# Kernel optimization log

Hardware: AMD Instinct MI355X
Metric: run time of the kernel (lower is better)

The kernel has to match this reference:

```python
import jax, jax.numpy as jnp
import numpy as np

WINDOW = 33  # must match init_kwargs window_size (odd)


def setup_inputs() -> dict:
    key = jax.random.key(0)
    kq, kk, kv, km = jax.random.split(key, 4)
    B, S, D = 4, 2048, 256
    query = jax.random.normal(kq, (B, S, D), dtype=jnp.float32)
    k = jax.random.normal(kk, (B, S, D), dtype=jnp.float32)
    value = jax.random.normal(kv, (B, S, D), dtype=jnp.float32)
    mask = jax.random.randint(km, (B, S), 0, 2).astype(jnp.int32)
    return {"query": query, "key": k, "value": value, "mask": mask}


def reference(query, key, value, mask):
    # Local (sliding-window) attention, window centered at each position.
    B, S, D = query.shape
    half = WINDOW // 2
    offs = jnp.arange(-half, half + 1)                 # [W]
    idx = jnp.arange(S)[:, None] + offs[None, :]       # [S, W]
    valid = (idx >= 0) & (idx < S)                     # in-bounds window entries
    idxc = jnp.clip(idx, 0, S - 1)
    k_win = key[:, idxc]                               # [B, S, W, D]
    v_win = value[:, idxc]                             # [B, S, W, D]
    scores = jnp.einsum('bsd,bswd->bsw', query, k_win) / jnp.sqrt(jnp.float32(D))
    m_win = (mask[:, idxc] != 0) & valid[None]         # [B, S, W]
    scores = jnp.where(m_win, scores, jnp.float32(-1e10))  # masked_fill(-1e10)
    p_attn = jax.nn.softmax(scores, axis=-1)           # [B, S, W]
    values = jnp.einsum('bsw,bswd->bsd', p_attn, v_win)
    return values, p_attn
```

## Files before the change

kernel.cpp:

```cpp
#include <hip/hip_runtime.h>

#define S_LEN 2048
#define D_DIM 256
#define WIN 33
#define HALF 16
#define TROWS 16
#define SPAN 48
#define SC_STRIDE 68
#define PT_STRIDE 72

typedef __attribute__((ext_vector_type(8))) short short8_t;
typedef __attribute__((ext_vector_type(4))) float f32x4;

__device__ inline unsigned pack2_bf16(float lo, float hi) {
    unsigned a = __float_as_uint(lo) + 0x8000u;
    unsigned b = __float_as_uint(hi) + 0x8000u;
    return __builtin_amdgcn_perm(b, a, 0x07060302);
}
__device__ inline short8_t pack_bf16x8(float4 x, float4 y) {
    union { unsigned u[4]; short8_t s; } r;
    r.u[0] = pack2_bf16(x.x, x.y); r.u[1] = pack2_bf16(x.z, x.w);
    r.u[2] = pack2_bf16(y.x, y.y); r.u[3] = pack2_bf16(y.z, y.w);
    return r.s;
}

__device__ inline void lds_barrier() {
    asm volatile("s_waitcnt lgkmcnt(0)\n\ts_barrier" ::: "memory");
}

__global__ __launch_bounds__(512, 4) void local_attn_v9(
    const float* __restrict__ q,
    const float* __restrict__ k,
    const float* __restrict__ v,
    const int*   __restrict__ mask,
    float* __restrict__ out_v,
    float* __restrict__ out_p)
{
    __shared__ __align__(16) float          Sc[2][TROWS * SC_STRIDE];
    __shared__ __align__(16) unsigned short Pt[TROWS * PT_STRIDE];
    __shared__ int wm[SPAN];

    const int t    = threadIdx.x;
    const int lane = t & 63;
    const int w    = t >> 6;
    const int l15  = lane & 15;
    const int q4   = lane >> 4;

    const int bid  = blockIdx.x;
    const int tile = ((bid & 7) << 6) | (bid >> 3);
    const int b    = tile >> 7;
    const int ts   = tile & 127;
    const int s0   = ts << 4;
    const bool interior = (ts >= 1) && (ts <= 126);

    const float* qb = q + ((size_t)b * S_LEN + s0) * D_DIM;
    const float* kb = k + (size_t)b * S_LEN * D_DIM;
    const float* vb = v + (size_t)b * S_LEN * D_DIM;

    if (t < SPAN) {
        const int idx = s0 - HALF + t;
        wm[t] = (idx >= 0 && idx < S_LEN) ? (mask[b * S_LEN + idx] != 0) : 0;
    }

    float vr[2][2][8];
    const bool act1 = (q4 < 2);

    if (interior) {
        if (w < 6) {
            const int tl = w >> 1;
            const int h  = w & 1;
            const int c  = 16 * tl + l15;
            const float* kr = kb + (size_t)(s0 - HALF + c) * D_DIM;
            const float* qr = qb + (size_t)l15 * D_DIM;
            f32x4 acc = (f32x4){0.f, 0.f, 0.f, 0.f};
#pragma unroll
            for (int i = 0; i < 4; ++i) {
                const int ks = 4 * h + i;
                const float* pq = qr + ks * 32 + q4 * 8;
                const float* pk = kr + ks * 32 + q4 * 8;
                const short8_t aq = pack_bf16x8(*(const float4*)pq, *(const float4*)(pq + 4));
                const short8_t bk = pack_bf16x8(*(const float4*)pk, *(const float4*)(pk + 4));
                acc = __builtin_amdgcn_mfma_f32_16x16x32_bf16(aq, bk, acc, 0, 0, 0);
            }
#pragma unroll
            for (int r = 0; r < 4; ++r)
                Sc[h][(q4 * 4 + r) * SC_STRIDE + c] = acc[r];
        }
        const float* pv = vb + (size_t)(s0 - HALF + q4 * 8) * D_DIM + 32 * w + l15;
#pragma unroll
        for (int nt = 0; nt < 2; ++nt) {
            const float* p0 = pv + nt * 16;
#pragma unroll
            for (int j = 0; j < 8; ++j)
                vr[nt][0][j] = p0[(size_t)j * D_DIM];
            if (act1) {
                const float* p1 = p0 + (size_t)32 * D_DIM;
#pragma unroll
                for (int j = 0; j < 8; ++j)
                    vr[nt][1][j] = p1[(size_t)j * D_DIM];
            }
        }
    } else {
        if (w < 6) {
            const int tl = w >> 1;
            const int h  = w & 1;
            const int c    = 16 * tl + l15;
            const int kidx = min(max(s0 - HALF + c, 0), S_LEN - 1);
            const float* kr = kb + (size_t)kidx * D_DIM;
            const float* qr = qb + (size_t)l15 * D_DIM;
            f32x4 acc = (f32x4){0.f, 0.f, 0.f, 0.f};
#pragma unroll
            for (int i = 0; i < 4; ++i) {
                const int ks = 4 * h + i;
                const float* pq = qr + ks * 32 + q4 * 8;
                const float* pk = kr + ks * 32 + q4 * 8;
                const short8_t aq = pack_bf16x8(*(const float4*)pq, *(const float4*)(pq + 4));
                const short8_t bk = pack_bf16x8(*(const float4*)pk, *(const float4*)(pk + 4));
                acc = __builtin_amdgcn_mfma_f32_16x16x32_bf16(aq, bk, acc, 0, 0, 0);
            }
#pragma unroll
            for (int r = 0; r < 4; ++r)
                Sc[h][(q4 * 4 + r) * SC_STRIDE + c] = acc[r];
        }
#pragma unroll
        for (int nt = 0; nt < 2; ++nt) {
            const int d = 32 * w + nt * 16 + l15;
#pragma unroll
            for (int j = 0; j < 8; ++j) {
                const int g0   = q4 * 8 + j;
                const int idx0 = min(max(s0 - HALF + g0, 0), S_LEN - 1);
                vr[nt][0][j] = vb[(size_t)idx0 * D_DIM + d];
            }
            if (act1) {
#pragma unroll
                for (int j = 0; j < 8; ++j) {
                    const int g1   = 32 + q4 * 8 + j;
                    const int idx1 = min(max(s0 - HALF + g1, 0), S_LEN - 1);
                    vr[nt][1][j] = vb[(size_t)idx1 * D_DIM + d];
                }
            }
        }
    }

    lds_barrier();

    {
        const int row = t >> 5;
        const int e   = t & 31;
        float vs[2];
#pragma unroll
        for (int kq = 0; kq < 2; ++kq) {
            const int c  = 2 * e + kq;
            const int j  = c - row;
            const int cc = (c < SPAN) ? c : 0;
            const bool inb = (j >= 0) && (j < WIN) && (c < SPAN);
            const float sv = (Sc[0][row * SC_STRIDE + cc] + Sc[1][row * SC_STRIDE + cc]) * 0.0625f;
            vs[kq] = inb ? (wm[cc] ? sv : -1e10f) : -1e30f;
        }
        float m = fmaxf(vs[0], vs[1]);
        m = fmaxf(m, __shfl_xor(m, 1, 64));
        m = fmaxf(m, __shfl_xor(m, 2, 64));
        m = fmaxf(m, __shfl_xor(m, 4, 64));
        m = fmaxf(m, __shfl_xor(m, 8, 64));
        m = fmaxf(m, __shfl_xor(m, 16, 64));
        float s = 0.f;
#pragma unroll
        for (int kq = 0; kq < 2; ++kq) { vs[kq] = __expf(vs[kq] - m); s += vs[kq]; }
        s += __shfl_xor(s, 1, 64);
        s += __shfl_xor(s, 2, 64);
        s += __shfl_xor(s, 4, 64);
        s += __shfl_xor(s, 8, 64);
        s += __shfl_xor(s, 16, 64);
        const float rinv = 1.0f / s;

        float p0 = vs[0] * rinv, p1 = vs[1] * rinv;
        *(unsigned*)&Pt[row * PT_STRIDE + 2 * e] = pack2_bf16(p0, p1);
        float* prow = out_p + ((size_t)(b * S_LEN + s0 + row)) * WIN;
        const int j0 = 2 * e - row;
        if (j0 >= 0 && j0 < WIN)         prow[j0]     = p0;
        if (j0 + 1 >= 0 && j0 + 1 < WIN) prow[j0 + 1] = p1;
    }

    lds_barrier();

    {
        const short8_t zfrag = {0, 0, 0, 0, 0, 0, 0, 0};
        short8_t bv[2][2];
#pragma unroll
        for (int nt = 0; nt < 2; ++nt) {
            float4 x, y;
            x.x = vr[nt][0][0]; x.y = vr[nt][0][1]; x.z = vr[nt][0][2]; x.w = vr[nt][0][3];
            y.x = vr[nt][0][4]; y.y = vr[nt][0][5]; y.z = vr[nt][0][6]; y.w = vr[nt][0][7];
            bv[nt][0] = pack_bf16x8(x, y);
            if (act1) {
                x.x = vr[nt][1][0]; x.y = vr[nt][1][1]; x.z = vr[nt][1][2]; x.w = vr[nt][1][3];
                y.x = vr[nt][1][4]; y.y = vr[nt][1][5]; y.z = vr[nt][1][6]; y.w = vr[nt][1][7];
                bv[nt][1] = pack_bf16x8(x, y);
            } else {
                bv[nt][1] = zfrag;
            }
        }

        const short8_t ap0 = *(const short8_t*)&Pt[l15 * PT_STRIDE + q4 * 8];
        const short8_t ap1 = *(const short8_t*)&Pt[l15 * PT_STRIDE + 32 + q4 * 8];
        float* ob = out_v + ((size_t)b * S_LEN + s0) * D_DIM;
#pragma unroll
        for (int nt = 0; nt < 2; ++nt) {
            f32x4 acc = (f32x4){0.f, 0.f, 0.f, 0.f};
            acc = __builtin_amdgcn_mfma_f32_16x16x32_bf16(ap0, bv[nt][0], acc, 0, 0, 0);
            acc = __builtin_amdgcn_mfma_f32_16x16x32_bf16(ap1, bv[nt][1], acc, 0, 0, 0);
            const int d = 32 * w + nt * 16 + l15;
#pragma unroll
            for (int r = 0; r < 4; ++r)
                ob[(size_t)(q4 * 4 + r) * D_DIM + d] = acc[r];
        }
    }
}

extern "C" void kernel_launch(void* const* d_in, const int* in_sizes, int n_in,
                              void* d_out, int out_size, void* d_ws, size_t ws_size,
                              hipStream_t stream) {
    const float* q    = (const float*)d_in[0];
    const float* k    = (const float*)d_in[1];
    const float* v    = (const float*)d_in[2];
    const int*   mask = (const int*)d_in[3];

    const int B = 4;
    float* out_v = (float*)d_out;
    float* out_p = (float*)d_out + (size_t)B * S_LEN * D_DIM;

    const int blocks = B * (S_LEN / TROWS);
    local_attn_v9<<<blocks, 512, 0, stream>>>(q, k, v, mask, out_v, out_p);
}
```

Baseline: 83.30 us.

## Process 32 query rows per block with 1024 threads to share K/V frame

```diff
diff --git a/kernel.cpp b/kernel.cpp
--- a/kernel.cpp
+++ b/kernel.cpp
@@ -4,8 +4,8 @@
 #define D_DIM 256
 #define WIN 33
 #define HALF 16
-#define TROWS 16
-#define SPAN 48
+#define TROWS 32
+#define FRAME 64
 #define SC_STRIDE 68
 #define PT_STRIDE 72
 
@@ -28,7 +28,7 @@
     asm volatile("s_waitcnt lgkmcnt(0)\n\ts_barrier" ::: "memory");
 }
 
-__global__ __launch_bounds__(512, 4) void local_attn_v9(
+__global__ __launch_bounds__(1024, 4) void local_attn_v10(
     const float* __restrict__ q,
     const float* __restrict__ k,
     const float* __restrict__ v,
@@ -38,7 +38,7 @@
 {
     __shared__ __align__(16) float          Sc[2][TROWS * SC_STRIDE];
     __shared__ __align__(16) unsigned short Pt[TROWS * PT_STRIDE];
-    __shared__ int wm[SPAN];
+    __shared__ int wm[FRAME];
 
     const int t    = threadIdx.x;
     const int lane = t & 63;
@@ -47,31 +47,33 @@
     const int q4   = lane >> 4;
 
     const int bid  = blockIdx.x;
-    const int tile = ((bid & 7) << 6) | (bid >> 3);
-    const int b    = tile >> 7;
-    const int ts   = tile & 127;
-    const int s0   = ts << 4;
-    const bool interior = (ts >= 1) && (ts <= 126);
+    const int tile = ((bid & 7) << 5) | (bid >> 3);
+    const int b    = tile >> 6;
+    const int ts   = tile & 63;
+    const int s0   = ts << 5;
+    const bool interior = (ts >= 1) && (ts <= 62);
 
     const float* qb = q + ((size_t)b * S_LEN + s0) * D_DIM;
     const float* kb = k + (size_t)b * S_LEN * D_DIM;
     const float* vb = v + (size_t)b * S_LEN * D_DIM;
 
-    if (t < SPAN) {
+    if (t < FRAME) {
         const int idx = s0 - HALF + t;
         wm[t] = (idx >= 0 && idx < S_LEN) ? (mask[b * S_LEN + idx] != 0) : 0;
     }
 
-    float vr[2][2][8];
-    const bool act1 = (q4 < 2);
+    const int tt = w >> 1;
+    const int h  = w & 1;
+    const int rt = tt >> 2;
+    const int ct = tt & 3;
+    const int c  = 16 * ct + l15;
+
+    float vr[2][8];
 
     if (interior) {
-        if (w < 6) {
-            const int tl = w >> 1;
-            const int h  = w & 1;
-            const int c  = 16 * tl + l15;
+        {
             const float* kr = kb + (size_t)(s0 - HALF + c) * D_DIM;
-            const float* qr = qb + (size_t)l15 * D_DIM;
+            const float* qr = qb + (size_t)(16 * rt + l15) * D_DIM;
             f32x4 acc = (f32x4){0.f, 0.f, 0.f, 0.f};
 #pragma unroll
             for (int i = 0; i < 4; ++i) {
@@ -84,30 +86,21 @@
             }
 #pragma unroll
             for (int r = 0; r < 4; ++r)
-                Sc[h][(q4 * 4 + r) * SC_STRIDE + c] = acc[r];
-        }
-        const float* pv = vb + (size_t)(s0 - HALF + q4 * 8) * D_DIM + 32 * w + l15;
-#pragma unroll
-        for (int nt = 0; nt < 2; ++nt) {
-            const float* p0 = pv + nt * 16;
-#pragma unroll
-            for (int j = 0; j < 8; ++j)
-                vr[nt][0][j] = p0[(size_t)j * D_DIM];
-            if (act1) {
-                const float* p1 = p0 + (size_t)32 * D_DIM;
-#pragma unroll
-                for (int j = 0; j < 8; ++j)
-                    vr[nt][1][j] = p1[(size_t)j * D_DIM];
-            }
-        }
+                Sc[h][(16 * rt + q4 * 4 + r) * SC_STRIDE + c] = acc[r];
+        }
+        const float* pv = vb + (size_t)(s0 - HALF + q4 * 8) * D_DIM + 16 * w + l15;
+#pragma unroll
+        for (int j = 0; j < 8; ++j)
+            vr[0][j] = pv[(size_t)j * D_DIM];
+        const float* pv1 = pv + (size_t)32 * D_DIM;
+#pragma unroll
+        for (int j = 0; j < 8; ++j)
+            vr[1][j] = pv1[(size_t)j * D_DIM];
     } else {
-        if (w < 6) {
-            const int tl = w >> 1;
-            const int h  = w & 1;
-            const int c    = 16 * tl + l15;
+        {
             const int kidx = min(max(s0 - HALF + c, 0), S_LEN - 1);
             const float* kr = kb + (size_t)kidx * D_DIM;
-            const float* qr = qb + (size_t)l15 * D_DIM;
+            const float* qr = qb + (size_t)(16 * rt + l15) * D_DIM;
             f32x4 acc = (f32x4){0.f, 0.f, 0.f, 0.f};
 #pragma unroll
             for (int i = 0; i < 4; ++i) {
@@ -120,26 +113,17 @@
             }
 #pragma unroll
             for (int r = 0; r < 4; ++r)
-                Sc[h][(q4 * 4 + r) * SC_STRIDE + c] = acc[r];
-        }
-#pragma unroll
-        for (int nt = 0; nt < 2; ++nt) {
-            const int d = 32 * w + nt * 16 + l15;
+                Sc[h][(16 * rt + q4 * 4 + r) * SC_STRIDE + c] = acc[r];
+        }
+        const int d = 16 * w + l15;
+#pragma unroll
+        for (int ks = 0; ks < 2; ++ks)
 #pragma unroll
             for (int j = 0; j < 8; ++j) {
-                const int g0   = q4 * 8 + j;
-                const int idx0 = min(max(s0 - HALF + g0, 0), S_LEN - 1);
-                vr[nt][0][j] = vb[(size_t)idx0 * D_DIM + d];
+                const int g   = ks * 32 + q4 * 8 + j;
+                const int idx = min(max(s0 - HALF + g, 0), S_LEN - 1);
+                vr[ks][j] = vb[(size_t)idx * D_DIM + d];
             }
-            if (act1) {
-#pragma unroll
-                for (int j = 0; j < 8; ++j) {
-                    const int g1   = 32 + q4 * 8 + j;
-                    const int idx1 = min(max(s0 - HALF + g1, 0), S_LEN - 1);
-                    vr[nt][1][j] = vb[(size_t)idx1 * D_DIM + d];
-                }
-            }
-        }
     }
 
     lds_barrier();
@@ -150,10 +134,9 @@
         float vs[2];
 #pragma unroll
         for (int kq = 0; kq < 2; ++kq) {
-            const int c  = 2 * e + kq;
-            const int j  = c - row;
-            const int cc = (c < SPAN) ? c : 0;
-            const bool inb = (j >= 0) && (j < WIN) && (c < SPAN);
+            const int cc = 2 * e + kq;
+            const int j  = cc - row;
+            const bool inb = (j >= 0) && (j < WIN);
             const float sv = (Sc[0][row * SC_STRIDE + cc] + Sc[1][row * SC_STRIDE + cc]) * 0.0625f;
             vs[kq] = inb ? (wm[cc] ? sv : -1e10f) : -1e30f;
         }
@@ -184,35 +167,27 @@
     lds_barrier();
 
     {
-        const short8_t zfrag = {0, 0, 0, 0, 0, 0, 0, 0};
-        short8_t bv[2][2];
-#pragma unroll
-        for (int nt = 0; nt < 2; ++nt) {
+        short8_t bv[2];
+#pragma unroll
+        for (int ks = 0; ks < 2; ++ks) {
             float4 x, y;
-            x.x = vr[nt][0][0]; x.y = vr[nt][0][1]; x.z = vr[nt][0][2]; x.w = vr[nt][0][3];
-            y.x = vr[nt][0][4]; y.y = vr[nt][0][5]; y.z = vr[nt][0][6]; y.w = vr[nt][0][7];
-            bv[nt][0] = pack_bf16x8(x, y);
-            if (act1) {
-                x.x = vr[nt][1][0]; x.y = vr[nt][1][1]; x.z = vr[nt][1][2]; x.w = vr[nt][1][3];
-                y.x = vr[nt][1][4]; y.y = vr[nt][1][5]; y.z = vr[nt][1][6]; y.w = vr[nt][1][7];
-                bv[nt][1] = pack_bf16x8(x, y);
-            } else {
-                bv[nt][1] = zfrag;
-            }
-        }
-
-        const short8_t ap0 = *(const short8_t*)&Pt[l15 * PT_STRIDE + q4 * 8];
-        const short8_t ap1 = *(const short8_t*)&Pt[l15 * PT_STRIDE + 32 + q4 * 8];
+            x.x = vr[ks][0]; x.y = vr[ks][1]; x.z = vr[ks][2]; x.w = vr[ks][3];
+            y.x = vr[ks][4]; y.y = vr[ks][5]; y.z = vr[ks][6]; y.w = vr[ks][7];
+            bv[ks] = pack_bf16x8(x, y);
+        }
+
         float* ob = out_v + ((size_t)b * S_LEN + s0) * D_DIM;
-#pragma unroll
-        for (int nt = 0; nt < 2; ++nt) {
+        const int d = 16 * w + l15;
+#pragma unroll
+        for (int rr = 0; rr < 2; ++rr) {
+            const short8_t ap0 = *(const short8_t*)&Pt[(16 * rr + l15) * PT_STRIDE + q4 * 8];
+            const short8_t ap1 = *(const short8_t*)&Pt[(16 * rr + l15) * PT_STRIDE + 32 + q4 * 8];
             f32x4 acc = (f32x4){0.f, 0.f, 0.f, 0.f};
-            acc = __builtin_amdgcn_mfma_f32_16x16x32_bf16(ap0, bv[nt][0], acc, 0, 0, 0);
-            acc = __builtin_amdgcn_mfma_f32_16x16x32_bf16(ap1, bv[nt][1], acc, 0, 0, 0);
-            const int d = 32 * w + nt * 16 + l15;
+            acc = __builtin_amdgcn_mfma_f32_16x16x32_bf16(ap0, bv[0], acc, 0, 0, 0);
+            acc = __builtin_amdgcn_mfma_f32_16x16x32_bf16(ap1, bv[1], acc, 0, 0, 0);
 #pragma unroll
             for (int r = 0; r < 4; ++r)
-                ob[(size_t)(q4 * 4 + r) * D_DIM + d] = acc[r];
+                ob[(size_t)(16 * rr + q4 * 4 + r) * D_DIM + d] = acc[r];
         }
     }
 }
@@ -230,5 +205,5 @@
     float* out_p = (float*)d_out + (size_t)B * S_LEN * D_DIM;
 
     const int blocks = B * (S_LEN / TROWS);
-    local_attn_v9<<<blocks, 512, 0, stream>>>(q, k, v, mask, out_v, out_p);
-}
+    local_attn_v10<<<blocks, 1024, 0, stream>>>(q, k, v, mask, out_v, out_p);
+}
```

After: 85.06 us. 2.1% more time.
